# Performance work log

Measured on AMD Instinct MI355X. Metric: run time of the kernel, lower is better.

Reference implementation:

```python
import jax, jax.numpy as jnp
import numpy as np

NEG_SLOPE = 0.2
LN_EPS = 1e-5
NUM_LAYERS = 4
H = 3            # num heads (both modalities)
C_MOL = 512      # molecule channels (in == out, required by the cat in forward)
C_PROT = 1280    # protein channels
VOCAB = 512 * 9 + 1
G_MOL = 512      # molecule graphs
G_PROT = 32      # protein graphs


def _with_self_loops(src, dst, n):
    loop = jnp.arange(n, dtype=src.dtype)
    return jnp.concatenate([src, loop]), jnp.concatenate([dst, loop])


def gat_conv(x, src, dst, W, a_src, a_dst, bias):
    """PyG GATConv, concat=False (head-mean), add_self_loops=True.
    x: [N, Fin], W: [Fin, H*C], a_src/a_dst: [H, C], bias: [C]."""
    n = x.shape[0]
    h = (x @ W).reshape(n, a_src.shape[0], a_src.shape[1])   # [N,H,C]
    al_s = jnp.sum(h * a_src, axis=-1)                       # [N,H]
    al_d = jnp.sum(h * a_dst, axis=-1)                       # [N,H]
    s, d = _with_self_loops(src, dst, n)
    e = jax.nn.leaky_relu(al_s[s] + al_d[d], NEG_SLOPE)      # [E+N,H]
    m = jax.ops.segment_max(e, d, num_segments=n)            # segment softmax (stable)
    m = jnp.where(jnp.isfinite(m), m, 0.0)
    p = jnp.exp(e - m[d])
    z = jax.ops.segment_sum(p, d, num_segments=n)
    alpha = p / (z[d] + 1e-16)                               # [E+N,H]
    out = jax.ops.segment_sum(h[s] * alpha[:, :, None], d, num_segments=n)  # [N,H,C]
    return out.mean(axis=1) + bias                           # concat=False -> head mean


def layer_norm(x, g, b):
    mu = x.mean(-1, keepdims=True)
    var = ((x - mu) ** 2).mean(-1, keepdims=True)
    return (x - mu) * jax.lax.rsqrt(var + LN_EPS) * g + b


def mean_pool(x, batch, num_graphs):
    s = jax.ops.segment_sum(x, batch, num_segments=num_graphs)
    cnt = jax.ops.segment_sum(jnp.ones((x.shape[0],), x.dtype), batch, num_segments=num_graphs)
    return s / jnp.maximum(cnt, 1.0)[:, None]


def setup_inputs() -> dict:
    key = jax.random.key(0)
    ks = jax.random.split(key, 20)
    n_mol, e_mol = 40000, 80000
    n_prot, e_prot = 8000, 64000
    drug_x = jax.random.randint(ks[0], (n_mol, 9), 0, VOCAB)
    mol_edge_index = jax.random.randint(ks[1], (2, e_mol), 0, n_mol)
    mol_batch = jnp.sort(jax.random.randint(ks[2], (n_mol,), 0, G_MOL))
    prot_x = jax.random.normal(ks[3], (n_prot, C_PROT), jnp.float32)
    prot_edge_index = jax.random.randint(ks[4], (2, e_prot), 0, n_prot)
    prot_batch = jnp.sort(jax.random.randint(ks[5], (n_prot,), 0, G_PROT))
    sc = 0.02
    emb = (jax.random.normal(ks[6], (VOCAB, C_MOL), jnp.float32) * sc).at[0].set(0.0)  # padding_idx=0
    mol_W = jax.random.normal(ks[7], (NUM_LAYERS, C_MOL, H * C_MOL), jnp.float32) * sc
    mol_asrc = jax.random.normal(ks[8], (NUM_LAYERS, H, C_MOL), jnp.float32) * sc
    mol_adst = jax.random.normal(ks[9], (NUM_LAYERS, H, C_MOL), jnp.float32) * sc
    mol_bias = jnp.zeros((NUM_LAYERS, C_MOL), jnp.float32)
    mol_ln_g = jnp.ones((NUM_LAYERS, C_MOL), jnp.float32)
    mol_ln_b = jnp.zeros((NUM_LAYERS, C_MOL), jnp.float32)
    prot_W = jax.random.normal(ks[10], (NUM_LAYERS, C_PROT, H * C_PROT), jnp.float32) * sc
    prot_asrc = jax.random.normal(ks[11], (NUM_LAYERS, H, C_PROT), jnp.float32) * sc
    prot_adst = jax.random.normal(ks[12], (NUM_LAYERS, H, C_PROT), jnp.float32) * sc
    prot_bias = jnp.zeros((NUM_LAYERS, C_PROT), jnp.float32)
    prot_ln_g = jnp.ones((NUM_LAYERS, C_PROT), jnp.float32)
    prot_ln_b = jnp.zeros((NUM_LAYERS, C_PROT), jnp.float32)
    return dict(drug_x=drug_x, mol_edge_index=mol_edge_index, mol_batch=mol_batch,
                prot_x=prot_x, prot_edge_index=prot_edge_index, prot_batch=prot_batch,
                emb=emb, mol_W=mol_W, mol_asrc=mol_asrc, mol_adst=mol_adst,
                mol_bias=mol_bias, mol_ln_g=mol_ln_g, mol_ln_b=mol_ln_b,
                prot_W=prot_W, prot_asrc=prot_asrc, prot_adst=prot_adst,
                prot_bias=prot_bias, prot_ln_g=prot_ln_g, prot_ln_b=prot_ln_b)


def reference(drug_x, mol_edge_index, mol_batch, prot_x, prot_edge_index, prot_batch,
              emb, mol_W, mol_asrc, mol_adst, mol_bias, mol_ln_g, mol_ln_b,
              prot_W, prot_asrc, prot_adst, prot_bias, prot_ln_g, prot_ln_b):
    # dropout layers are identity (eval mode)
    mol_x = emb[drug_x].mean(axis=-2)                       # [N_mol, C_MOL]
    mol_feats = [mean_pool(mol_x, mol_batch, G_MOL)]
    prot_feats = [mean_pool(prot_x, prot_batch, G_PROT)]
    msrc, mdst = mol_edge_index[0], mol_edge_index[1]
    psrc, pdst = prot_edge_index[0], prot_edge_index[1]
    px = prot_x
    for i in range(NUM_LAYERS):
        mol_x = gat_conv(mol_x, msrc, mdst, mol_W[i], mol_asrc[i], mol_adst[i], mol_bias[i])
        mol_x = layer_norm(mol_x, mol_ln_g[i], mol_ln_b[i])
        px = gat_conv(px, psrc, pdst, prot_W[i], prot_asrc[i], prot_adst[i], prot_bias[i])
        px = layer_norm(px, prot_ln_g[i], prot_ln_b[i])
        mol_feats.append(mean_pool(mol_x, mol_batch, G_MOL))
        prot_feats.append(mean_pool(px, prot_batch, G_PROT))
    return jnp.stack(mol_feats, axis=1), jnp.stack(prot_feats, axis=1)  # [G,5,C] each
```

## Files before the change

### kernel.cpp

```cpp
#include <hip/hip_runtime.h>
#include <cstdint>


constexpr int H_HEADS = 3;
constexpr float NEG_SLOPE = 0.2f;
constexpr float LN_EPS = 1e-5f;
constexpr int N_MOL = 40000, E_MOL = 80000, C_MOL = 512, G_MOL = 512;
constexpr int N_PROT = 8000, E_PROT = 64000, C_PROT = 1280, G_PROT = 32;
constexpr int LAYERS = 4;
constexpr int MPAD_MOL = 40064;
constexpr int MPAD_PROT = 8064;

typedef unsigned short u16;
typedef __attribute__((ext_vector_type(8))) short short8v;
typedef __attribute__((ext_vector_type(4))) unsigned short ushort4v;
typedef __attribute__((ext_vector_type(4))) float f32x4;

__device__ __forceinline__ float bf2f(u16 s) {
    union { unsigned u; float f; } v; v.u = ((unsigned)s) << 16; return v.f;
}
__device__ __forceinline__ u16 f2bf(float f) {
    union { float f; unsigned u; } v; v.f = f;
    return (u16)((v.u + 0x7fffu + ((v.u >> 16) & 1u)) >> 16);
}

__device__ __forceinline__ void g2l16(const void* g, void* l) {
    __builtin_amdgcn_global_load_lds((const __attribute__((address_space(1))) void*)g,
                                     (__attribute__((address_space(3))) void*)l, 16, 0, 0);
}


__global__ void set_int_kernel(int* p, int v, int n) {
    int i = blockIdx.x * blockDim.x + threadIdx.x;
    if (i < n) p[i] = v;
}

__global__ void zero_f32_kernel(float* p, int n) {
    int i = blockIdx.x * blockDim.x + threadIdx.x;
    if (i < n) p[i] = 0.f;
}

__global__ void copy_int_kernel(const int* __restrict__ s, int* __restrict__ d, int n) {
    int i = blockIdx.x * blockDim.x + threadIdx.x;
    if (i < n) d[i] = s[i];
}

__global__ void hist_kernel(const int* __restrict__ keys, int n, int* __restrict__ cnt) {
    int i = blockIdx.x * blockDim.x + threadIdx.x;
    if (i < n) atomicAdd(&cnt[keys[i]], 1);
}

__global__ void scan_kernel(const int* __restrict__ in, int* __restrict__ out, int n) {
    __shared__ int sums[1024];
    const int t = threadIdx.x;
    const int chunk = (n + 1023) / 1024;
    const int start = t * chunk;
    const int end = min(start + chunk, n);
    int s = 0;
    for (int i = start; i < end; ++i) s += in[i];
    sums[t] = s;
    __syncthreads();
    if (t == 0) {
        int acc = 0;
        for (int i = 0; i < 1024; ++i) { int v = sums[i]; sums[i] = acc; acc += v; }
        out[n] = acc;
    }
    __syncthreads();
    int acc = sums[t];
    for (int i = start; i < end; ++i) { out[i] = acc; acc += in[i]; }
}

__global__ void fill_self_kernel(int* __restrict__ pos, int* __restrict__ srcl, int n) {
    int i = blockIdx.x * blockDim.x + threadIdx.x;
    if (i < n) { int slot = atomicAdd(&pos[i], 1); srcl[slot] = i; }
}

__global__ void fill_edge_kernel(const int* __restrict__ src, const int* __restrict__ dst, int e,
                                 int* __restrict__ pos, int* __restrict__ srcl) {
    int i = blockIdx.x * blockDim.x + threadIdx.x;
    if (i < e) { int slot = atomicAdd(&pos[dst[i]], 1); srcl[slot] = src[i]; }
}

__global__ void f32_to_bf16(const float* __restrict__ in, u16* __restrict__ out, int n) {
    int i = blockIdx.x * blockDim.x + threadIdx.x;
    if (i < n) out[i] = f2bf(in[i]);
}


__global__ void embed_mean_kernel(const int* __restrict__ drug_x, const float* __restrict__ emb,
                                  u16* __restrict__ out) {
    const int n = blockIdx.x;
    __shared__ int idx[9];
    if (threadIdx.x < 9) idx[threadIdx.x] = drug_x[n * 9 + threadIdx.x];
    __syncthreads();
    const int c = threadIdx.x;
    float s = 0.f;
#pragma unroll
    for (int t = 0; t < 9; ++t) s += emb[(size_t)idx[t] * C_MOL + c];
    out[(size_t)n * C_MOL + c] = f2bf(s * (1.f / 9.f));
}


__global__ __launch_bounds__(256) void transfold(const float* __restrict__ W, u16* __restrict__ Wt,
                                                 const float* __restrict__ asrc,
                                                 const float* __restrict__ adst,
                                                 float* __restrict__ wsrc, float* __restrict__ wdst,
                                                 int CIN, int COUT, size_t headStride, int ldn) {
    __shared__ float t[32][33];
    __shared__ float rs[8][33], rd[8][33];
    const int h = blockIdx.z;
    const int n0 = blockIdx.x * 32, k0 = blockIdx.y * 32;
    const int tx = threadIdx.x & 31, ty = threadIdx.x >> 5;
#pragma unroll
    for (int q = 0; q < 4; ++q)
        t[ty + q * 8][tx] = W[(size_t)(k0 + ty + q * 8) * (H_HEADS * COUT) + h * COUT + n0 + tx];
    __syncthreads();
#pragma unroll
    for (int q = 0; q < 4; ++q)
        Wt[(size_t)h * headStride + (size_t)(n0 + ty + q * 8) * ldn + k0 + tx] =
            f2bf(t[tx][ty + q * 8]);
    float ps = 0.f, pd = 0.f;
    const float* as = asrc + h * COUT + n0;
    const float* ad = adst + h * COUT + n0;
#pragma unroll
    for (int q = 0; q < 4; ++q) {
        const float w = t[tx][ty + q * 8];
        ps += w * as[ty + q * 8];
        pd += w * ad[ty + q * 8];
    }
    rs[ty][tx] = ps;
    rd[ty][tx] = pd;
    __syncthreads();
    if (ty == 0) {
        float s = 0.f, d = 0.f;
#pragma unroll
        for (int j = 0; j < 8; ++j) { s += rs[j][tx]; d += rd[j][tx]; }
        atomicAdd(&wsrc[h * CIN + k0 + tx], s);
        atomicAdd(&wdst[h * CIN + k0 + tx], d);
    }
}


template <int C>
__global__ void attn_logits(const u16* __restrict__ x, const float* __restrict__ wsrc,
                            const float* __restrict__ wdst, float* __restrict__ als,
                            float* __restrict__ ald) {
    constexpr int PER = C / 64;
    const int n = blockIdx.x, lane = threadIdx.x;
    const u16* xr = x + (size_t)n * C + lane * PER;
    float xv[PER];
#pragma unroll
    for (int i = 0; i < PER; i += 4) {
        const ushort4v v = *(const ushort4v*)(xr + i);
        xv[i] = bf2f(v.x); xv[i + 1] = bf2f(v.y); xv[i + 2] = bf2f(v.z); xv[i + 3] = bf2f(v.w);
    }
    for (int h = 0; h < H_HEADS; ++h) {
        const float* ws = wsrc + h * C + lane * PER;
        const float* wd = wdst + h * C + lane * PER;
        float ss = 0.f, sd = 0.f;
#pragma unroll
        for (int i = 0; i < PER; i += 4) {
            const float4 a = *(const float4*)(ws + i);
            const float4 b = *(const float4*)(wd + i);
            ss += xv[i] * a.x + xv[i + 1] * a.y + xv[i + 2] * a.z + xv[i + 3] * a.w;
            sd += xv[i] * b.x + xv[i + 1] * b.y + xv[i + 2] * b.z + xv[i + 3] * b.w;
        }
        for (int o = 32; o; o >>= 1) { ss += __shfl_down(ss, o); sd += __shfl_down(sd, o); }
        if (lane == 0) { als[n * H_HEADS + h] = ss; ald[n * H_HEADS + h] = sd; }
    }
}


__device__ __forceinline__ void agg_mol_part(const u16* __restrict__ x,
                                             const float* __restrict__ als,
                                             const float* __restrict__ ald,
                                             const int* __restrict__ indptr,
                                             const int* __restrict__ srcl, u16* __restrict__ agg,
                                             float* smem) {
    constexpr int MAXD = 128;
    const int wv = threadIdx.x >> 6, lane = threadIdx.x & 63;
    const int n = blockIdx.x * 5 + wv;
    const int beg = indptr[n], end = indptr[n + 1];
    const int deg = end - beg;
    float* atab = smem + wv * (MAXD * 3);
    float m = -1e30f, zi = 0.f;
    if (lane < H_HEADS) {
        const float ad = ald[n * H_HEADS + lane];
        for (int e = beg; e < end; ++e) {
            float v = als[srcl[e] * H_HEADS + lane] + ad;
            v = v >= 0.f ? v : NEG_SLOPE * v;
            m = fmaxf(m, v);
        }
        float z = 0.f;
        for (int e = beg; e < end; ++e) {
            float v = als[srcl[e] * H_HEADS + lane] + ad;
            v = v >= 0.f ? v : NEG_SLOPE * v;
            z += __expf(v - m);
        }
        zi = 1.f / (z + 1e-16f);
    }
    const float m0 = __shfl(m, 0), m1 = __shfl(m, 1), m2 = __shfl(m, 2);
    const float z0 = __shfl(zi, 0), z1 = __shfl(zi, 1), z2 = __shfl(zi, 2);
    const float ad0 = ald[n * H_HEADS + 0], ad1 = ald[n * H_HEADS + 1], ad2 = ald[n * H_HEADS + 2];
    const bool fits = deg <= MAXD;
    if (fits) {
        for (int i = lane; i < deg * 3; i += 64) {
            const int e = i / 3, h = i - e * 3;
            float v = als[srcl[beg + e] * H_HEADS + h] + (h == 0 ? ad0 : (h == 1 ? ad1 : ad2));
            v = v >= 0.f ? v : NEG_SLOPE * v;
            const float mh = h == 0 ? m0 : (h == 1 ? m1 : m2);
            const float zh = h == 0 ? z0 : (h == 1 ? z1 : z2);
            atab[i] = __expf(v - mh) * zh;
        }
    }
    __syncthreads();
    float acc[H_HEADS][8];
#pragma unroll
    for (int h = 0; h < H_HEADS; ++h)
#pragma unroll
        for (int j = 0; j < 8; ++j) acc[h][j] = 0.f;
    for (int e = 0; e < deg; ++e) {
        const int s = srcl[beg + e];
        float a0, a1, a2;
        if (fits) {
            a0 = atab[e * 3 + 0]; a1 = atab[e * 3 + 1]; a2 = atab[e * 3 + 2];
        } else {
            float v0 = als[s * H_HEADS + 0] + ad0; v0 = v0 >= 0.f ? v0 : NEG_SLOPE * v0;
            float v1 = als[s * H_HEADS + 1] + ad1; v1 = v1 >= 0.f ? v1 : NEG_SLOPE * v1;
            float v2 = als[s * H_HEADS + 2] + ad2; v2 = v2 >= 0.f ? v2 : NEG_SLOPE * v2;
            a0 = __expf(v0 - m0) * z0; a1 = __expf(v1 - m1) * z1; a2 = __expf(v2 - m2) * z2;
        }
        const short8v row = *(const short8v*)(x + (size_t)s * C_MOL + lane * 8);
#pragma unroll
        for (int j = 0; j < 8; ++j) {
            const float f = bf2f((u16)row[j]);
            acc[0][j] += a0 * f; acc[1][j] += a1 * f; acc[2][j] += a2 * f;
        }
    }
    u16* o = agg + (size_t)n * (3 * C_MOL) + lane * 8;
#pragma unroll
    for (int h = 0; h < H_HEADS; ++h) {
        short8v r;
#pragma unroll
        for (int j = 0; j < 8; ++j) r[j] = (short)f2bf(acc[h][j]);
        *(short8v*)(o + h * C_MOL) = r;
    }
}

__device__ __forceinline__ void agg_prot_part(const u16* __restrict__ x,
                                              const float* __restrict__ als,
                                              const float* __restrict__ ald,
                                              const int* __restrict__ indptr,
                                              const int* __restrict__ srcl, u16* __restrict__ agg,
                                              float* smem, int n) {
    constexpr int MAXD = 500;
    const int tid = threadIdx.x;
    const int beg = indptr[n], end = indptr[n + 1];
    const int deg = end - beg;
    float* mz = smem;
    float* atab = smem + 6;
    if (tid < H_HEADS) {
        const float ad = ald[n * H_HEADS + tid];
        float m = -1e30f;
        for (int e = beg; e < end; ++e) {
            float v = als[srcl[e] * H_HEADS + tid] + ad;
            v = v >= 0.f ? v : NEG_SLOPE * v;
            m = fmaxf(m, v);
        }
        float z = 0.f;
        for (int e = beg; e < end; ++e) {
            float v = als[srcl[e] * H_HEADS + tid] + ad;
            v = v >= 0.f ? v : NEG_SLOPE * v;
            z += __expf(v - m);
        }
        mz[tid] = m;
        mz[3 + tid] = 1.f / (z + 1e-16f);
    }
    __syncthreads();
    const bool fits = deg <= MAXD;
    if (fits) {
        for (int i = tid; i < deg * 3; i += 320) {
            const int e = i / 3, h = i - e * 3;
            float v = als[srcl[beg + e] * H_HEADS + h] + ald[n * H_HEADS + h];
            v = v >= 0.f ? v : NEG_SLOPE * v;
            atab[i] = __expf(v - mz[h]) * mz[3 + h];
        }
    }
    __syncthreads();
    const float m0 = mz[0], m1 = mz[1], m2 = mz[2];
    const float z0 = mz[3], z1 = mz[4], z2 = mz[5];
    const float ad0 = ald[n * H_HEADS + 0], ad1 = ald[n * H_HEADS + 1], ad2 = ald[n * H_HEADS + 2];
    float acc[H_HEADS][4];
#pragma unroll
    for (int h = 0; h < H_HEADS; ++h)
#pragma unroll
        for (int j = 0; j < 4; ++j) acc[h][j] = 0.f;
    for (int e = 0; e < deg; ++e) {
        const int s = srcl[beg + e];
        float a0, a1, a2;
        if (fits) {
            a0 = atab[e * 3 + 0]; a1 = atab[e * 3 + 1]; a2 = atab[e * 3 + 2];
        } else {
            float v0 = als[s * H_HEADS + 0] + ad0; v0 = v0 >= 0.f ? v0 : NEG_SLOPE * v0;
            float v1 = als[s * H_HEADS + 1] + ad1; v1 = v1 >= 0.f ? v1 : NEG_SLOPE * v1;
            float v2 = als[s * H_HEADS + 2] + ad2; v2 = v2 >= 0.f ? v2 : NEG_SLOPE * v2;
            a0 = __expf(v0 - m0) * z0; a1 = __expf(v1 - m1) * z1; a2 = __expf(v2 - m2) * z2;
        }
        const ushort4v v = *(const ushort4v*)(x + (size_t)s * C_PROT + tid * 4);
        const float f0 = bf2f(v.x), f1 = bf2f(v.y), f2 = bf2f(v.z), f3 = bf2f(v.w);
        acc[0][0] += a0 * f0; acc[0][1] += a0 * f1; acc[0][2] += a0 * f2; acc[0][3] += a0 * f3;
        acc[1][0] += a1 * f0; acc[1][1] += a1 * f1; acc[1][2] += a1 * f2; acc[1][3] += a1 * f3;
        acc[2][0] += a2 * f0; acc[2][1] += a2 * f1; acc[2][2] += a2 * f2; acc[2][3] += a2 * f3;
    }
    u16* o = agg + (size_t)n * (3 * C_PROT) + tid * 4;
#pragma unroll
    for (int h = 0; h < H_HEADS; ++h) {
        ushort4v r;
        r.x = f2bf(acc[h][0]); r.y = f2bf(acc[h][1]); r.z = f2bf(acc[h][2]); r.w = f2bf(acc[h][3]);
        *(ushort4v*)(o + h * C_PROT) = r;
    }
}

__global__ __launch_bounds__(320) void agg_both(
    const u16* __restrict__ xM, const float* __restrict__ alsM, const float* __restrict__ aldM,
    const int* __restrict__ iptrM, const int* __restrict__ srclM, u16* __restrict__ aggM,
    const u16* __restrict__ xP, const float* __restrict__ alsP, const float* __restrict__ aldP,
    const int* __restrict__ iptrP, const int* __restrict__ srclP, u16* __restrict__ aggP,
    int molBlocks) {
    __shared__ float smem[1920];
    if ((int)blockIdx.x < molBlocks)
        agg_mol_part(xM, alsM, aldM, iptrM, srclM, aggM, smem);
    else
        agg_prot_part(xP, alsP, aldP, iptrP, srclP, aggP, smem, blockIdx.x - molBlocks);
}


__global__ __launch_bounds__(256) void gemm128d(
    const u16* __restrict__ A0, const u16* __restrict__ B0, u16* __restrict__ C0,
    int N0, int K0, int nx0, int M0, int g0,
    const u16* __restrict__ A1, const u16* __restrict__ B1, u16* __restrict__ C1,
    int N1, int K1, int nx1, int M1) {
    __shared__ u16 lds[16384];
    const int tid = threadIdx.x;
    const int w = tid >> 6, l = tid & 63;
    const int wr = w >> 1, wc = w & 1;

    const int bid = blockIdx.x;
    const u16 *A, *Bt;
    u16* Cout;
    int N, K, nxch, Mreal, base, sz;
    if (bid < g0) { base = 0; sz = g0; A = A0; Bt = B0; Cout = C0; N = N0; K = K0; nxch = nx0; Mreal = M0; }
    else { base = g0; sz = gridDim.x - g0; A = A1; Bt = B1; Cout = C1; N = N1; K = K1; nxch = nx1; Mreal = M1; }
    const int j = bid - base;
    const int q = sz >> 3, r = sz & 7;
    const int xcd = j & 7, idx = j >> 3;
    const int wg = (xcd < r ? xcd * (q + 1) : r * (q + 1) + (xcd - r) * q) + idx;
    const int nx = wg % nxch, my = wg / nxch;
    const size_t bm = (size_t)my * 128, bn = (size_t)nx * 128;

    const f32x4 zf = {0.f, 0.f, 0.f, 0.f};
    f32x4 acc[4][4];
#pragma unroll
    for (int i = 0; i < 4; ++i)
#pragma unroll
        for (int jj = 0; jj < 4; ++jj) acc[i][jj] = zf;

    const int srow = w * 32 + (l >> 3);
    const int sseg = (l & 7) ^ (l >> 3);
    const u16* Ab = A + (bm + srow) * (size_t)K + sseg * 8;
    const u16* Bb = Bt + (bn + srow) * (size_t)K + sseg * 8;

    for (int k0 = 0; k0 < K; k0 += 64) {
#pragma unroll
        for (int qq = 0; qq < 4; ++qq)
            g2l16(Ab + k0 + (size_t)qq * 8 * K, lds + (w * 4 + qq) * 512);
#pragma unroll
        for (int qq = 0; qq < 4; ++qq)
            g2l16(Bb + k0 + (size_t)qq * 8 * K, lds + 8192 + (w * 4 + qq) * 512);
        __syncthreads();
#pragma unroll
        for (int kk = 0; kk < 2; ++kk) {
            const int sg = ((kk * 4 + (l >> 4)) ^ (l & 7)) * 8;
            short8v af[4], bf8[4];
#pragma unroll
            for (int fm = 0; fm < 4; ++fm) {
                const int row = wr * 64 + fm * 16 + (l & 15);
                af[fm] = *(const short8v*)&lds[row * 64 + sg];
            }
#pragma unroll
            for (int fn = 0; fn < 4; ++fn) {
                const int row = wc * 64 + fn * 16 + (l & 15);
                bf8[fn] = *(const short8v*)&lds[8192 + row * 64 + sg];
            }
#pragma unroll
            for (int fm = 0; fm < 4; ++fm)
#pragma unroll
                for (int fn = 0; fn < 4; ++fn)
                    acc[fm][fn] = __builtin_amdgcn_mfma_f32_16x16x32_bf16(af[fm], bf8[fn],
                                                                          acc[fm][fn], 0, 0, 0);
        }
        __syncthreads();
    }

#pragma unroll
    for (int half = 0; half < 2; ++half) {
        if (wr == half) {
#pragma unroll
            for (int fm = 0; fm < 4; ++fm)
#pragma unroll
                for (int fn = 0; fn < 4; ++fn) {
                    const int col = wc * 64 + fn * 16 + (l & 15);
#pragma unroll
                    for (int rr = 0; rr < 4; ++rr)
                        lds[(fm * 16 + (l >> 4) * 4 + rr) * 136 + col] = f2bf(acc[fm][fn][rr]);
                }
        }
        __syncthreads();
        const int lrow = tid >> 2, lseg = tid & 3;
        const size_t grow = bm + half * 64 + lrow;
        if (grow < (size_t)Mreal) {
            u16* Crow = Cout + grow * (size_t)N + bn + lseg * 32;
            const u16* Lr = lds + lrow * 136 + lseg * 32;
#pragma unroll
            for (int ii = 0; ii < 4; ++ii)
                *(float4*)(Crow + ii * 8) = *(const float4*)(Lr + ii * 8);
        }
        __syncthreads();
    }
}


template <int C, int LOGITS>
__global__ __launch_bounds__(C / 4) void ln_kernel(u16* __restrict__ x,
                                                   const float* __restrict__ bias,
                                                   const float* __restrict__ g,
                                                   const float* __restrict__ b,
                                                   const float* __restrict__ wsrc_n,
                                                   const float* __restrict__ wdst_n,
                                                   float* __restrict__ als,
                                                   float* __restrict__ ald) {
    constexpr int NT = C / 4;
    constexpr int NW = NT / 64;
    const int n = blockIdx.x, tid = threadIdx.x;
    u16* xr = x + (size_t)n * C + tid * 4;
    constexpr float invH = 1.f / (float)H_HEADS;
    const ushort4v xv = *(const ushort4v*)xr;
    const float4 bi = *(const float4*)(bias + tid * 4);
    const float v0 = bf2f(xv.x) * invH + bi.x;
    const float v1 = bf2f(xv.y) * invH + bi.y;
    const float v2 = bf2f(xv.z) * invH + bi.z;
    const float v3 = bf2f(xv.w) * invH + bi.w;
    float s1 = v0 + v1 + v2 + v3;
    float s2 = v0 * v0 + v1 * v1 + v2 * v2 + v3 * v3;
    __shared__ float red[2][NW];
    __shared__ float red2[NW][6];
    for (int o = 32; o; o >>= 1) { s1 += __shfl_down(s1, o); s2 += __shfl_down(s2, o); }
    if ((tid & 63) == 0) { red[0][tid >> 6] = s1; red[1][tid >> 6] = s2; }
    __syncthreads();
    float t1 = 0.f, t2 = 0.f;
#pragma unroll
    for (int i = 0; i < NW; ++i) { t1 += red[0][i]; t2 += red[1][i]; }
    const float mu = t1 / C;
    const float var = t2 / C - mu * mu;
    const float rstd = rsqrtf(var + LN_EPS);
    const float4 gg = *(const float4*)(g + tid * 4);
    const float4 bb = *(const float4*)(b + tid * 4);
    ushort4v ov;
    ov.x = f2bf((v0 - mu) * rstd * gg.x + bb.x);
    ov.y = f2bf((v1 - mu) * rstd * gg.y + bb.y);
    ov.z = f2bf((v2 - mu) * rstd * gg.z + bb.z);
    ov.w = f2bf((v3 - mu) * rstd * gg.w + bb.w);
    *(ushort4v*)xr = ov;
    if (LOGITS) {
        const float q0 = bf2f(ov.x), q1 = bf2f(ov.y), q2 = bf2f(ov.z), q3 = bf2f(ov.w);
        float ps[3], pd[3];
#pragma unroll
        for (int h = 0; h < 3; ++h) {
            const float4 a = *(const float4*)(wsrc_n + h * C + tid * 4);
            const float4 d = *(const float4*)(wdst_n + h * C + tid * 4);
            ps[h] = q0 * a.x + q1 * a.y + q2 * a.z + q3 * a.w;
            pd[h] = q0 * d.x + q1 * d.y + q2 * d.z + q3 * d.w;
        }
        for (int o = 32; o; o >>= 1) {
#pragma unroll
            for (int h = 0; h < 3; ++h) {
                ps[h] += __shfl_down(ps[h], o);
                pd[h] += __shfl_down(pd[h], o);
            }
        }
        if ((tid & 63) == 0) {
            const int wv = tid >> 6;
#pragma unroll
            for (int h = 0; h < 3; ++h) { red2[wv][h] = ps[h]; red2[wv][3 + h] = pd[h]; }
        }
        __syncthreads();
        if (tid == 0) {
#pragma unroll
            for (int h = 0; h < 3; ++h) {
                float as = 0.f, ad = 0.f;
#pragma unroll
                for (int i = 0; i < NW; ++i) { as += red2[i][h]; ad += red2[i][3 + h]; }
                als[n * H_HEADS + h] = as;
                ald[n * H_HEADS + h] = ad;
            }
        }
    }
}


template <int C, int S>
__global__ void pool_atomic(const u16* __restrict__ x, const int* __restrict__ goff,
                            float* __restrict__ out, int layer) {
    const int g = blockIdx.x, seg = blockIdx.y;
    const int beg = goff[g], end = goff[g + 1];
    const int len = end - beg;
    const int s0 = beg + (len * seg) / S;
    const int s1 = beg + (len * (seg + 1)) / S;
    if (s0 >= s1) return;
    const float inv = 1.f / fmaxf((float)len, 1.f);
    const int tid = threadIdx.x;
    float a0 = 0.f, a1 = 0.f, a2 = 0.f, a3 = 0.f;
    for (int n = s0; n < s1; ++n) {
        const ushort4v v = *(const ushort4v*)(x + (size_t)n * C + tid * 4);
        a0 += bf2f(v.x); a1 += bf2f(v.y); a2 += bf2f(v.z); a3 += bf2f(v.w);
    }
    float* o = out + ((size_t)g * (LAYERS + 1) + layer) * C + tid * 4;
    atomicAdd(o + 0, a0 * inv);
    atomicAdd(o + 1, a1 * inv);
    atomicAdd(o + 2, a2 * inv);
    atomicAdd(o + 3, a3 * inv);
}


extern "C" void kernel_launch(void* const* d_in, const int* in_sizes, int n_in, void* d_out,
                              int out_size, void* d_ws, size_t ws_size, hipStream_t stream) {
    const int* drug_x      = (const int*)d_in[0];
    const int* mol_ei      = (const int*)d_in[1];
    const int* mol_batch   = (const int*)d_in[2];
    const float* prot_in   = (const float*)d_in[3];
    const int* prot_ei     = (const int*)d_in[4];
    const int* prot_batch  = (const int*)d_in[5];
    const float* emb       = (const float*)d_in[6];
    const float* mol_W     = (const float*)d_in[7];
    const float* mol_asrc  = (const float*)d_in[8];
    const float* mol_adst  = (const float*)d_in[9];
    const float* mol_bias  = (const float*)d_in[10];
    const float* mol_lng   = (const float*)d_in[11];
    const float* mol_lnb   = (const float*)d_in[12];
    const float* prot_W    = (const float*)d_in[13];
    const float* prot_asrc = (const float*)d_in[14];
    const float* prot_adst = (const float*)d_in[15];
    const float* prot_bias = (const float*)d_in[16];
    const float* prot_lng  = (const float*)d_in[17];
    const float* prot_lnb  = (const float*)d_in[18];

    if (ws_size < (size_t)262000000) return;

    char* base = (char*)d_ws;
    size_t off = 0;
    auto alloc = [&](size_t bytes) -> void* {
        void* r = base + off;
        off = (off + bytes + 255) & ~(size_t)255;
        return r;
    };
    u16* x_mol  = (u16*)alloc((size_t)N_MOL * C_MOL * 2);
    u16* x_prot = (u16*)alloc((size_t)N_PROT * C_PROT * 2);
    u16* aggM   = (u16*)alloc((size_t)3 * MPAD_MOL * C_MOL * 2);
    u16* WtM    = (u16*)alloc((size_t)H_HEADS * C_MOL * C_MOL * 2);
    u16* WtP    = (u16*)alloc((size_t)H_HEADS * C_PROT * C_PROT * 2);
    u16* aggP   = (u16*)alloc((size_t)3 * MPAD_PROT * C_PROT * 2);
    float* wsrcM = (float*)alloc((size_t)LAYERS * H_HEADS * C_MOL * 4);
    float* wdstM = (float*)alloc((size_t)LAYERS * H_HEADS * C_MOL * 4);
    float* wsrcP = (float*)alloc((size_t)LAYERS * H_HEADS * C_PROT * 4);
    float* wdstP = (float*)alloc((size_t)LAYERS * H_HEADS * C_PROT * 4);
    float* alsM = (float*)alloc((size_t)N_MOL * H_HEADS * 4);
    float* aldM = (float*)alloc((size_t)N_MOL * H_HEADS * 4);
    float* alsP = (float*)alloc((size_t)N_PROT * H_HEADS * 4);
    float* aldP = (float*)alloc((size_t)N_PROT * H_HEADS * 4);
    int* mol_indptr  = (int*)alloc((N_MOL + 1) * 4);
    int* mol_pos     = (int*)alloc(N_MOL * 4);
    int* mol_srcl    = (int*)alloc((E_MOL + N_MOL) * 4);
    int* prot_indptr = (int*)alloc((N_PROT + 1) * 4);
    int* prot_pos    = (int*)alloc(N_PROT * 4);
    int* prot_srcl   = (int*)alloc((E_PROT + N_PROT) * 4);
    int* cnt         = (int*)alloc(N_MOL * 4);
    int* mol_goff    = (int*)alloc((G_MOL + 1) * 4);
    int* prot_goff   = (int*)alloc((G_PROT + 1) * 4);
    int* gcnt        = (int*)alloc(G_MOL * 4);

    float* out_mol  = (float*)d_out;
    float* out_prot = (float*)d_out + (size_t)G_MOL * (LAYERS + 1) * C_MOL;

    zero_f32_kernel<<<(out_size + 255) / 256, 256, 0, stream>>>((float*)d_out, out_size);
    zero_f32_kernel<<<(LAYERS * H_HEADS * C_MOL + 255) / 256, 256, 0, stream>>>(
        wsrcM, LAYERS * H_HEADS * C_MOL);
    zero_f32_kernel<<<(LAYERS * H_HEADS * C_MOL + 255) / 256, 256, 0, stream>>>(
        wdstM, LAYERS * H_HEADS * C_MOL);
    zero_f32_kernel<<<(LAYERS * H_HEADS * C_PROT + 255) / 256, 256, 0, stream>>>(
        wsrcP, LAYERS * H_HEADS * C_PROT);
    zero_f32_kernel<<<(LAYERS * H_HEADS * C_PROT + 255) / 256, 256, 0, stream>>>(
        wdstP, LAYERS * H_HEADS * C_PROT);

    set_int_kernel<<<(N_MOL + 255) / 256, 256, 0, stream>>>(cnt, 1, N_MOL);
    hist_kernel<<<(E_MOL + 255) / 256, 256, 0, stream>>>(mol_ei + E_MOL, E_MOL, cnt);
    scan_kernel<<<1, 1024, 0, stream>>>(cnt, mol_indptr, N_MOL);
    copy_int_kernel<<<(N_MOL + 255) / 256, 256, 0, stream>>>(mol_indptr, mol_pos, N_MOL);
    fill_self_kernel<<<(N_MOL + 255) / 256, 256, 0, stream>>>(mol_pos, mol_srcl, N_MOL);
    fill_edge_kernel<<<(E_MOL + 255) / 256, 256, 0, stream>>>(mol_ei, mol_ei + E_MOL, E_MOL, mol_pos,
                                                              mol_srcl);
    set_int_kernel<<<(N_PROT + 255) / 256, 256, 0, stream>>>(cnt, 1, N_PROT);
    hist_kernel<<<(E_PROT + 255) / 256, 256, 0, stream>>>(prot_ei + E_PROT, E_PROT, cnt);
    scan_kernel<<<1, 1024, 0, stream>>>(cnt, prot_indptr, N_PROT);
    copy_int_kernel<<<(N_PROT + 255) / 256, 256, 0, stream>>>(prot_indptr, prot_pos, N_PROT);
    fill_self_kernel<<<(N_PROT + 255) / 256, 256, 0, stream>>>(prot_pos, prot_srcl, N_PROT);
    fill_edge_kernel<<<(E_PROT + 255) / 256, 256, 0, stream>>>(prot_ei, prot_ei + E_PROT, E_PROT,
                                                               prot_pos, prot_srcl);

    set_int_kernel<<<(G_MOL + 255) / 256, 256, 0, stream>>>(gcnt, 0, G_MOL);
    hist_kernel<<<(N_MOL + 255) / 256, 256, 0, stream>>>(mol_batch, N_MOL, gcnt);
    scan_kernel<<<1, 1024, 0, stream>>>(gcnt, mol_goff, G_MOL);
    set_int_kernel<<<(G_PROT + 255) / 256, 256, 0, stream>>>(gcnt, 0, G_PROT);
    hist_kernel<<<(N_PROT + 255) / 256, 256, 0, stream>>>(prot_batch, N_PROT, gcnt);
    scan_kernel<<<1, 1024, 0, stream>>>(gcnt, prot_goff, G_PROT);

    transfold<<<dim3(C_MOL / 32, C_MOL / 32, H_HEADS), 256, 0, stream>>>(
        mol_W, WtM, mol_asrc, mol_adst, wsrcM, wdstM, C_MOL, C_MOL, (size_t)C_MOL, 3 * C_MOL);
    transfold<<<dim3(C_PROT / 32, C_PROT / 32, H_HEADS), 256, 0, stream>>>(
        prot_W, WtP, prot_asrc, prot_adst, wsrcP, wdstP, C_PROT, C_PROT, (size_t)C_PROT,
        3 * C_PROT);

    f32_to_bf16<<<(N_PROT * C_PROT + 255) / 256, 256, 0, stream>>>(prot_in, x_prot, N_PROT * C_PROT);
    embed_mean_kernel<<<N_MOL, C_MOL, 0, stream>>>(drug_x, emb, x_mol);
    pool_atomic<C_MOL, 8><<<dim3(G_MOL, 8), C_MOL / 4, 0, stream>>>(x_mol, mol_goff, out_mol, 0);
    pool_atomic<C_PROT, 64><<<dim3(G_PROT, 64), C_PROT / 4, 0, stream>>>(x_prot, prot_goff,
                                                                         out_prot, 0);
    attn_logits<C_MOL><<<N_MOL, 64, 0, stream>>>(x_mol, wsrcM, wdstM, alsM, aldM);
    attn_logits<C_PROT><<<N_PROT, 64, 0, stream>>>(x_prot, wsrcP, wdstP, alsP, aldP);

    const int gMol = (MPAD_MOL / 128) * (C_MOL / 128);
    const int gProt = (MPAD_PROT / 128) * (C_PROT / 128);
    const int molAggBlocks = N_MOL / 5;

    for (int l = 0; l < LAYERS; ++l) {
        const int last = (l == LAYERS - 1);
        agg_both<<<molAggBlocks + N_PROT, 320, 0, stream>>>(
            x_mol, alsM, aldM, mol_indptr, mol_srcl, aggM,
            x_prot, alsP, aldP, prot_indptr, prot_srcl, aggP, molAggBlocks);
        gemm128d<<<gProt + gMol, 256, 0, stream>>>(
            aggP, WtP, x_prot, C_PROT, 3 * C_PROT, C_PROT / 128, N_PROT, gProt,
            aggM, WtM, x_mol, C_MOL, 3 * C_MOL, C_MOL / 128, N_MOL);
        if (!last) {
            transfold<<<dim3(C_MOL / 32, C_MOL / 32, H_HEADS), 256, 0, stream>>>(
                mol_W + (size_t)(l + 1) * C_MOL * (H_HEADS * C_MOL), WtM,
                mol_asrc + (size_t)(l + 1) * H_HEADS * C_MOL,
                mol_adst + (size_t)(l + 1) * H_HEADS * C_MOL,
                wsrcM + (size_t)(l + 1) * H_HEADS * C_MOL,
                wdstM + (size_t)(l + 1) * H_HEADS * C_MOL, C_MOL, C_MOL, (size_t)C_MOL,
                3 * C_MOL);
            transfold<<<dim3(C_PROT / 32, C_PROT / 32, H_HEADS), 256, 0, stream>>>(
                prot_W + (size_t)(l + 1) * C_PROT * (H_HEADS * C_PROT), WtP,
                prot_asrc + (size_t)(l + 1) * H_HEADS * C_PROT,
                prot_adst + (size_t)(l + 1) * H_HEADS * C_PROT,
                wsrcP + (size_t)(l + 1) * H_HEADS * C_PROT,
                wdstP + (size_t)(l + 1) * H_HEADS * C_PROT, C_PROT, C_PROT, (size_t)C_PROT,
                3 * C_PROT);
            ln_kernel<C_MOL, 1><<<N_MOL, C_MOL / 4, 0, stream>>>(
                x_mol, mol_bias + (size_t)l * C_MOL, mol_lng + (size_t)l * C_MOL,
                mol_lnb + (size_t)l * C_MOL, wsrcM + (size_t)(l + 1) * H_HEADS * C_MOL,
                wdstM + (size_t)(l + 1) * H_HEADS * C_MOL, alsM, aldM);
            ln_kernel<C_PROT, 1><<<N_PROT, C_PROT / 4, 0, stream>>>(
                x_prot, prot_bias + (size_t)l * C_PROT, prot_lng + (size_t)l * C_PROT,
                prot_lnb + (size_t)l * C_PROT, wsrcP + (size_t)(l + 1) * H_HEADS * C_PROT,
                wdstP + (size_t)(l + 1) * H_HEADS * C_PROT, alsP, aldP);
        } else {
            ln_kernel<C_MOL, 0><<<N_MOL, C_MOL / 4, 0, stream>>>(
                x_mol, mol_bias + (size_t)l * C_MOL, mol_lng + (size_t)l * C_MOL,
                mol_lnb + (size_t)l * C_MOL, nullptr, nullptr, nullptr, nullptr);
            ln_kernel<C_PROT, 0><<<N_PROT, C_PROT / 4, 0, stream>>>(
                x_prot, prot_bias + (size_t)l * C_PROT, prot_lng + (size_t)l * C_PROT,
                prot_lnb + (size_t)l * C_PROT, nullptr, nullptr, nullptr, nullptr);
        }
        pool_atomic<C_MOL, 8><<<dim3(G_MOL, 8), C_MOL / 4, 0, stream>>>(x_mol, mol_goff, out_mol,
                                                                        l + 1);
        pool_atomic<C_PROT, 64><<<dim3(G_PROT, 64), C_PROT / 4, 0, stream>>>(x_prot, prot_goff,
                                                                             out_prot, l + 1);
    }
}
```

Before: 2.253 ms.

## Cache leaky logits in LDS, merge pooling launches, bf16 embedding gather

```diff
diff --git a/kernel.cpp b/kernel.cpp
--- a/kernel.cpp
+++ b/kernel.cpp
@@ -10,6 +10,7 @@
 constexpr int LAYERS = 4;
 constexpr int MPAD_MOL = 40064;
 constexpr int MPAD_PROT = 8064;
+constexpr int VOCAB = 512 * 9 + 1;
 
 typedef unsigned short u16;
 typedef __attribute__((ext_vector_type(8))) short short8v;
@@ -87,17 +88,24 @@
 }
 
 
-__global__ void embed_mean_kernel(const int* __restrict__ drug_x, const float* __restrict__ emb,
-                                  u16* __restrict__ out) {
+__global__ __launch_bounds__(128) void embed_mean_v(const int* __restrict__ drug_x,
+                                                    const u16* __restrict__ emb_bf,
+                                                    u16* __restrict__ out) {
     const int n = blockIdx.x;
     __shared__ int idx[9];
     if (threadIdx.x < 9) idx[threadIdx.x] = drug_x[n * 9 + threadIdx.x];
     __syncthreads();
-    const int c = threadIdx.x;
-    float s = 0.f;
-#pragma unroll
-    for (int t = 0; t < 9; ++t) s += emb[(size_t)idx[t] * C_MOL + c];
-    out[(size_t)n * C_MOL + c] = f2bf(s * (1.f / 9.f));
+    const int c4 = threadIdx.x * 4;
+    float a0 = 0.f, a1 = 0.f, a2 = 0.f, a3 = 0.f;
+#pragma unroll
+    for (int t = 0; t < 9; ++t) {
+        const ushort4v v = *(const ushort4v*)(emb_bf + (size_t)idx[t] * C_MOL + c4);
+        a0 += bf2f(v.x); a1 += bf2f(v.y); a2 += bf2f(v.z); a3 += bf2f(v.w);
+    }
+    ushort4v r;
+    r.x = f2bf(a0 * (1.f / 9.f)); r.y = f2bf(a1 * (1.f / 9.f));
+    r.z = f2bf(a2 * (1.f / 9.f)); r.w = f2bf(a3 * (1.f / 9.f));
+    *(ushort4v*)(out + (size_t)n * C_MOL + c4) = r;
 }
 
 
@@ -183,34 +191,46 @@
     const int beg = indptr[n], end = indptr[n + 1];
     const int deg = end - beg;
     float* atab = smem + wv * (MAXD * 3);
-    float m = -1e30f, zi = 0.f;
-    if (lane < H_HEADS) {
-        const float ad = ald[n * H_HEADS + lane];
-        for (int e = beg; e < end; ++e) {
-            float v = als[srcl[e] * H_HEADS + lane] + ad;
-            v = v >= 0.f ? v : NEG_SLOPE * v;
-            m = fmaxf(m, v);
-        }
-        float z = 0.f;
-        for (int e = beg; e < end; ++e) {
-            float v = als[srcl[e] * H_HEADS + lane] + ad;
-            v = v >= 0.f ? v : NEG_SLOPE * v;
-            z += __expf(v - m);
-        }
-        zi = 1.f / (z + 1e-16f);
-    }
-    const float m0 = __shfl(m, 0), m1 = __shfl(m, 1), m2 = __shfl(m, 2);
-    const float z0 = __shfl(zi, 0), z1 = __shfl(zi, 1), z2 = __shfl(zi, 2);
     const float ad0 = ald[n * H_HEADS + 0], ad1 = ald[n * H_HEADS + 1], ad2 = ald[n * H_HEADS + 2];
     const bool fits = deg <= MAXD;
     if (fits) {
         for (int i = lane; i < deg * 3; i += 64) {
             const int e = i / 3, h = i - e * 3;
             float v = als[srcl[beg + e] * H_HEADS + h] + (h == 0 ? ad0 : (h == 1 ? ad1 : ad2));
-            v = v >= 0.f ? v : NEG_SLOPE * v;
-            const float mh = h == 0 ? m0 : (h == 1 ? m1 : m2);
-            const float zh = h == 0 ? z0 : (h == 1 ? z1 : z2);
-            atab[i] = __expf(v - mh) * zh;
+            atab[i] = v >= 0.f ? v : NEG_SLOPE * v;
+        }
+    }
+    __syncthreads();
+    float m = -1e30f, zi = 0.f;
+    if (lane < H_HEADS) {
+        if (fits) {
+            for (int e = 0; e < deg; ++e) m = fmaxf(m, atab[e * 3 + lane]);
+            float z = 0.f;
+            for (int e = 0; e < deg; ++e) z += __expf(atab[e * 3 + lane] - m);
+            zi = 1.f / (z + 1e-16f);
+        } else {
+            const float ad = lane == 0 ? ad0 : (lane == 1 ? ad1 : ad2);
+            for (int e = beg; e < end; ++e) {
+                float v = als[srcl[e] * H_HEADS + lane] + ad;
+                v = v >= 0.f ? v : NEG_SLOPE * v;
+                m = fmaxf(m, v);
+            }
+            float z = 0.f;
+            for (int e = beg; e < end; ++e) {
+                float v = als[srcl[e] * H_HEADS + lane] + ad;
+                v = v >= 0.f ? v : NEG_SLOPE * v;
+                z += __expf(v - m);
+            }
+            zi = 1.f / (z + 1e-16f);
+        }
+    }
+    const float m0 = __shfl(m, 0), m1 = __shfl(m, 1), m2 = __shfl(m, 2);
+    const float z0 = __shfl(zi, 0), z1 = __shfl(zi, 1), z2 = __shfl(zi, 2);
+    if (fits) {
+        for (int i = lane; i < deg * 3; i += 64) {
+            const int h = i - (i / 3) * 3;
+            atab[i] = __expf(atab[i] - (h == 0 ? m0 : (h == 1 ? m1 : m2))) *
+                      (h == 0 ? z0 : (h == 1 ? z1 : z2));
         }
     }
     __syncthreads();
@@ -259,37 +279,48 @@
     const int deg = end - beg;
     float* mz = smem;
     float* atab = smem + 6;
-    if (tid < H_HEADS) {
-        const float ad = ald[n * H_HEADS + tid];
-        float m = -1e30f;
-        for (int e = beg; e < end; ++e) {
-            float v = als[srcl[e] * H_HEADS + tid] + ad;
-            v = v >= 0.f ? v : NEG_SLOPE * v;
-            m = fmaxf(m, v);
-        }
-        float z = 0.f;
-        for (int e = beg; e < end; ++e) {
-            float v = als[srcl[e] * H_HEADS + tid] + ad;
-            v = v >= 0.f ? v : NEG_SLOPE * v;
-            z += __expf(v - m);
-        }
-        mz[tid] = m;
-        mz[3 + tid] = 1.f / (z + 1e-16f);
-    }
-    __syncthreads();
+    const float ad0 = ald[n * H_HEADS + 0], ad1 = ald[n * H_HEADS + 1], ad2 = ald[n * H_HEADS + 2];
     const bool fits = deg <= MAXD;
     if (fits) {
         for (int i = tid; i < deg * 3; i += 320) {
             const int e = i / 3, h = i - e * 3;
-            float v = als[srcl[beg + e] * H_HEADS + h] + ald[n * H_HEADS + h];
-            v = v >= 0.f ? v : NEG_SLOPE * v;
-            atab[i] = __expf(v - mz[h]) * mz[3 + h];
-        }
+            float v = als[srcl[beg + e] * H_HEADS + h] + (h == 0 ? ad0 : (h == 1 ? ad1 : ad2));
+            atab[i] = v >= 0.f ? v : NEG_SLOPE * v;
+        }
+    }
+    __syncthreads();
+    if (tid < H_HEADS) {
+        float m = -1e30f, z = 0.f;
+        if (fits) {
+            for (int e = 0; e < deg; ++e) m = fmaxf(m, atab[e * 3 + tid]);
+            for (int e = 0; e < deg; ++e) z += __expf(atab[e * 3 + tid] - m);
+        } else {
+            const float ad = tid == 0 ? ad0 : (tid == 1 ? ad1 : ad2);
+            for (int e = beg; e < end; ++e) {
+                float v = als[srcl[e] * H_HEADS + tid] + ad;
+                v = v >= 0.f ? v : NEG_SLOPE * v;
+                m = fmaxf(m, v);
+            }
+            for (int e = beg; e < end; ++e) {
+                float v = als[srcl[e] * H_HEADS + tid] + ad;
+                v = v >= 0.f ? v : NEG_SLOPE * v;
+                z += __expf(v - m);
+            }
+        }
+        mz[tid] = m;
+        mz[3 + tid] = 1.f / (z + 1e-16f);
     }
     __syncthreads();
     const float m0 = mz[0], m1 = mz[1], m2 = mz[2];
     const float z0 = mz[3], z1 = mz[4], z2 = mz[5];
-    const float ad0 = ald[n * H_HEADS + 0], ad1 = ald[n * H_HEADS + 1], ad2 = ald[n * H_HEADS + 2];
+    if (fits) {
+        for (int i = tid; i < deg * 3; i += 320) {
+            const int h = i - (i / 3) * 3;
+            atab[i] = __expf(atab[i] - (h == 0 ? m0 : (h == 1 ? m1 : m2))) *
+                      (h == 0 ? z0 : (h == 1 ? z1 : z2));
+        }
+    }
+    __syncthreads();
     float acc[H_HEADS][4];
 #pragma unroll
     for (int h = 0; h < H_HEADS; ++h)
@@ -508,27 +539,54 @@
 }
 
 
-template <int C, int S>
-__global__ void pool_atomic(const u16* __restrict__ x, const int* __restrict__ goff,
-                            float* __restrict__ out, int layer) {
-    const int g = blockIdx.x, seg = blockIdx.y;
-    const int beg = goff[g], end = goff[g + 1];
-    const int len = end - beg;
-    const int s0 = beg + (len * seg) / S;
-    const int s1 = beg + (len * (seg + 1)) / S;
-    if (s0 >= s1) return;
-    const float inv = 1.f / fmaxf((float)len, 1.f);
+__global__ __launch_bounds__(320) void pool_both(const u16* __restrict__ xM,
+                                                 const int* __restrict__ goffM,
+                                                 float* __restrict__ outM,
+                                                 const u16* __restrict__ xP,
+                                                 const int* __restrict__ goffP,
+                                                 float* __restrict__ outP, int layer,
+                                                 int molBlocks) {
+    const int b = blockIdx.x;
     const int tid = threadIdx.x;
-    float a0 = 0.f, a1 = 0.f, a2 = 0.f, a3 = 0.f;
-    for (int n = s0; n < s1; ++n) {
-        const ushort4v v = *(const ushort4v*)(x + (size_t)n * C + tid * 4);
-        a0 += bf2f(v.x); a1 += bf2f(v.y); a2 += bf2f(v.z); a3 += bf2f(v.w);
-    }
-    float* o = out + ((size_t)g * (LAYERS + 1) + layer) * C + tid * 4;
-    atomicAdd(o + 0, a0 * inv);
-    atomicAdd(o + 1, a1 * inv);
-    atomicAdd(o + 2, a2 * inv);
-    atomicAdd(o + 3, a3 * inv);
+    if (b < molBlocks) {
+        if (tid >= C_MOL / 4) return;
+        const int g = b >> 3, seg = b & 7;
+        const int beg = goffM[g], end = goffM[g + 1];
+        const int len = end - beg;
+        const int s0 = beg + (len * seg) / 8;
+        const int s1 = beg + (len * (seg + 1)) / 8;
+        if (s0 >= s1) return;
+        const float inv = 1.f / fmaxf((float)len, 1.f);
+        float a0 = 0.f, a1 = 0.f, a2 = 0.f, a3 = 0.f;
+        for (int n = s0; n < s1; ++n) {
+            const ushort4v v = *(const ushort4v*)(xM + (size_t)n * C_MOL + tid * 4);
+            a0 += bf2f(v.x); a1 += bf2f(v.y); a2 += bf2f(v.z); a3 += bf2f(v.w);
+        }
+        float* o = outM + ((size_t)g * (LAYERS + 1) + layer) * C_MOL + tid * 4;
+        atomicAdd(o + 0, a0 * inv);
+        atomicAdd(o + 1, a1 * inv);
+        atomicAdd(o + 2, a2 * inv);
+        atomicAdd(o + 3, a3 * inv);
+    } else {
+        const int bb = b - molBlocks;
+        const int g = bb >> 6, seg = bb & 63;
+        const int beg = goffP[g], end = goffP[g + 1];
+        const int len = end - beg;
+        const int s0 = beg + (len * seg) / 64;
+        const int s1 = beg + (len * (seg + 1)) / 64;
+        if (s0 >= s1) return;
+        const float inv = 1.f / fmaxf((float)len, 1.f);
+        float a0 = 0.f, a1 = 0.f, a2 = 0.f, a3 = 0.f;
+        for (int n = s0; n < s1; ++n) {
+            const ushort4v v = *(const ushort4v*)(xP + (size_t)n * C_PROT + tid * 4);
+            a0 += bf2f(v.x); a1 += bf2f(v.y); a2 += bf2f(v.z); a3 += bf2f(v.w);
+        }
+        float* o = outP + ((size_t)g * (LAYERS + 1) + layer) * C_PROT + tid * 4;
+        atomicAdd(o + 0, a0 * inv);
+        atomicAdd(o + 1, a1 * inv);
+        atomicAdd(o + 2, a2 * inv);
+        atomicAdd(o + 3, a3 * inv);
+    }
 }
 
 
@@ -588,6 +646,8 @@
     int* prot_goff   = (int*)alloc((G_PROT + 1) * 4);
     int* gcnt        = (int*)alloc(G_MOL * 4);
 
+    u16* emb_bf = aggM;
+
     float* out_mol  = (float*)d_out;
     float* out_prot = (float*)d_out + (size_t)G_MOL * (LAYERS + 1) * C_MOL;
 
@@ -629,11 +689,11 @@
         prot_W, WtP, prot_asrc, prot_adst, wsrcP, wdstP, C_PROT, C_PROT, (size_t)C_PROT,
         3 * C_PROT);
 
+    f32_to_bf16<<<(VOCAB * C_MOL + 255) / 256, 256, 0, stream>>>(emb, emb_bf, VOCAB * C_MOL);
     f32_to_bf16<<<(N_PROT * C_PROT + 255) / 256, 256, 0, stream>>>(prot_in, x_prot, N_PROT * C_PROT);
-    embed_mean_kernel<<<N_MOL, C_MOL, 0, stream>>>(drug_x, emb, x_mol);
-    pool_atomic<C_MOL, 8><<<dim3(G_MOL, 8), C_MOL / 4, 0, stream>>>(x_mol, mol_goff, out_mol, 0);
-    pool_atomic<C_PROT, 64><<<dim3(G_PROT, 64), C_PROT / 4, 0, stream>>>(x_prot, prot_goff,
-                                                                         out_prot, 0);
+    embed_mean_v<<<N_MOL, 128, 0, stream>>>(drug_x, emb_bf, x_mol);
+    pool_both<<<G_MOL * 8 + G_PROT * 64, 320, 0, stream>>>(x_mol, mol_goff, out_mol, x_prot,
+                                                           prot_goff, out_prot, 0, G_MOL * 8);
     attn_logits<C_MOL><<<N_MOL, 64, 0, stream>>>(x_mol, wsrcM, wdstM, alsM, aldM);
     attn_logits<C_PROT><<<N_PROT, 64, 0, stream>>>(x_prot, wsrcP, wdstP, alsP, aldP);
 
@@ -680,9 +740,8 @@
                 x_prot, prot_bias + (size_t)l * C_PROT, prot_lng + (size_t)l * C_PROT,
                 prot_lnb + (size_t)l * C_PROT, nullptr, nullptr, nullptr, nullptr);
         }
-        pool_atomic<C_MOL, 8><<<dim3(G_MOL, 8), C_MOL / 4, 0, stream>>>(x_mol, mol_goff, out_mol,
-                                                                        l + 1);
-        pool_atomic<C_PROT, 64><<<dim3(G_PROT, 64), C_PROT / 4, 0, stream>>>(x_prot, prot_goff,
-                                                                             out_prot, l + 1);
-    }
-}
+        pool_both<<<G_MOL * 8 + G_PROT * 64, 320, 0, stream>>>(x_mol, mol_goff, out_mol, x_prot,
+                                                               prot_goff, out_prot, l + 1,
+                                                               G_MOL * 8);
+    }
+}
```

After: 2.049 ms. 9.1% less time.
